# Performance work log

Measured on AMD Instinct MI355X. Metric: run time of the kernel, lower is better.

The kernel has to match this reference:

```python
import jax, jax.numpy as jnp
import numpy as np

N_NODES = 100000
N_EDGES = 1000000
D_FEAT = 64          # per-node embedding dim
IN_FEATS = 2 * D_FEAT  # concat(src, dst)
HID = 128


def setup_inputs() -> dict:
    key = jax.random.key(0)
    ks = jax.random.split(key, 12)
    zi = jax.random.normal(ks[0], (N_NODES, D_FEAT), dtype=jnp.float32)
    zj = jax.random.normal(ks[1], (N_NODES, D_FEAT), dtype=jnp.float32)
    zn = jax.random.normal(ks[2], (N_NODES, D_FEAT), dtype=jnp.float32)
    pos_src = jax.random.randint(ks[3], (N_EDGES,), 0, N_NODES)
    pos_dst = jax.random.randint(ks[4], (N_EDGES,), 0, N_NODES)
    neg_src = jax.random.randint(ks[5], (N_EDGES,), 0, N_NODES)
    neg_dst = jax.random.randint(ks[6], (N_EDGES,), 0, N_NODES)
    # MLP params (nn.Linear style: y = x @ W.T + b)
    s1 = 1.0 / np.sqrt(IN_FEATS)
    s3 = 1.0 / np.sqrt(HID)
    W1 = jax.random.uniform(ks[7], (HID, IN_FEATS), jnp.float32, -s1, s1)
    b1 = jax.random.uniform(ks[8], (HID,), jnp.float32, -s1, s1)
    W3 = jax.random.uniform(ks[9], (1, HID), jnp.float32, -s3, s3)
    b3 = jax.random.uniform(ks[10], (1,), jnp.float32, -s3, s3)
    return {"zi": zi, "zj": zj, "zn": zn, "W1": W1, "b1": b1, "W3": W3,
            "b3": b3, "pos_src": pos_src, "pos_dst": pos_dst,
            "neg_src": neg_src, "neg_dst": neg_dst}


def _lp(raw, W1, b1, W3, b3):
    # Link_Prediction with n_layers=2, dropout=0: linear-relu-linear-sigmoid
    hid = jax.nn.relu(raw @ W1.T + b1)      # [E, HID]
    return jax.nn.sigmoid(hid @ W3.T + b3)  # [E, 1]


def reference(zi, zj, zn, W1, b1, W3, b3, pos_src, pos_dst, neg_src, neg_dst):
    # pos graph: gather src/dst node embeddings per edge, concat -> MLP
    raw_pos = jnp.concatenate([zi[pos_src], zj[pos_dst]], axis=1)  # [E, 2*D]
    pos_score = _lp(raw_pos, W1, b1, W3, b3)
    # NOTE: source bug — neg score is computed from the POS raw features
    # (pos_graph.edata['raw']); the neg gather/concat is dead code, so we
    # faithfully score raw_pos again.
    neg_score = _lp(raw_pos, W1, b1, W3, b3)
    return pos_score, neg_score
```

## Files before the change

### kernel.cpp

```cpp
#include <hip/hip_runtime.h>
#include <hip/hip_fp8.h>

typedef float    f32x16 __attribute__((ext_vector_type(16)));
typedef _Float16 f16x8  __attribute__((ext_vector_type(8)));
typedef long     i64;

#define NWAVES 4
#define TPW 4
#define TILES_PER_BLOCK (NWAVES * TPW)
#define W1_LDS 32768

__device__ __forceinline__ uint32_t enc4_fp8(float a, float b, float c, float d) {
#if __has_builtin(__builtin_amdgcn_cvt_pk_fp8_f32)
    int w = __builtin_amdgcn_cvt_pk_fp8_f32(a, b, 0, false);
    w     = __builtin_amdgcn_cvt_pk_fp8_f32(c, d, w, true);
    return (uint32_t)w;
#else
    __hip_fp8_e4m3 e0(a), e1(b), e2(c), e3(d);
    return (uint32_t)e0.__x | ((uint32_t)e1.__x << 8) |
           ((uint32_t)e2.__x << 16) | ((uint32_t)e3.__x << 24);
#endif
}

__device__ __forceinline__ void dec4_fp8f(uint32_t w, float* o) {
#if __has_builtin(__builtin_amdgcn_cvt_pk_f32_fp8)
    const auto f01 = __builtin_amdgcn_cvt_pk_f32_fp8((int)w, false);
    const auto f23 = __builtin_amdgcn_cvt_pk_f32_fp8((int)w, true);
    o[0] = f01[0]; o[1] = f01[1]; o[2] = f23[0]; o[3] = f23[1];
#else
    #pragma unroll
    for (int j = 0; j < 4; ++j) {
        __hip_fp8_e4m3 t; t.__x = (unsigned char)(w >> (8 * j));
        o[j] = (float)t;
    }
#endif
}

__device__ __forceinline__ i64 mk64(uint32_t lo, uint32_t hi) {
    return (i64)(((unsigned long long)hi << 32) | (unsigned long long)lo);
}

__device__ __forceinline__ void gl_lds16(const void* g, void* l) {
    __builtin_amdgcn_global_load_lds(
        (const __attribute__((address_space(1))) void*)g,
        (__attribute__((address_space(3))) void*)l, 16, 0, 0);
}

__global__ __launch_bounds__(256) void prep_fp8(
    const float* __restrict__ zi, const float* __restrict__ zj,
    uint2* __restrict__ zif8, uint2* __restrict__ zjf8, const int nChunkPer)
{
    const int stride = gridDim.x * blockDim.x;
    for (int c = blockIdx.x * blockDim.x + threadIdx.x; c < 2 * nChunkPer; c += stride) {
        const float* s;
        uint2* d;
        int cc;
        if (c < nChunkPer) { cc = c; s = zi + (size_t)cc * 8; d = zif8 + cc; }
        else { cc = c - nChunkPer; s = zj + (size_t)cc * 8; d = zjf8 + cc; }
        const float4 a0 = *reinterpret_cast<const float4*>(s);
        const float4 a1 = *reinterpret_cast<const float4*>(s + 4);
        uint2 w;
        w.x = enc4_fp8(a0.x, a0.y, a0.z, a0.w);
        w.y = enc4_fp8(a1.x, a1.y, a1.z, a1.w);
        *d = w;
    }
}

__global__ __launch_bounds__(256) void prep_w1(
    const float* __restrict__ W1, uint4* __restrict__ w1pack)
{
    const int c = blockIdx.x * blockDim.x + threadIdx.x;
    if (c >= 2048) return;
    const int n  = c >> 4, q = c & 15;
    const int kk = q >> 1, lq = q & 1;
    const int kbase = (kk < 4) ? (lq * 32 + kk * 8) : (64 + lq * 32 + (kk - 4) * 8);
    const float* w = W1 + n * 128 + kbase;
    const float4 w0 = *reinterpret_cast<const float4*>(w);
    const float4 w1 = *reinterpret_cast<const float4*>(w + 4);
    const uint32_t h0 = enc4_fp8(w0.x, w0.y, w0.z, w0.w);
    const uint32_t h1 = enc4_fp8(w1.x, w1.y, w1.z, w1.w);
    float d0[4], d1[4];
    dec4_fp8f(h0, d0);
    dec4_fp8f(h1, d1);
    const uint32_t r0 = enc4_fp8((w0.x - d0[0]) * 16.0f, (w0.y - d0[1]) * 16.0f,
                                 (w0.z - d0[2]) * 16.0f, (w0.w - d0[3]) * 16.0f);
    const uint32_t r1 = enc4_fp8((w1.x - d1[0]) * 16.0f, (w1.y - d1[1]) * 16.0f,
                                 (w1.z - d1[2]) * 16.0f, (w1.w - d1[3]) * 16.0f);
    uint4 o; o.x = h0; o.y = h1; o.z = r0; o.w = r1;
    w1pack[c] = o;
}

template<bool FP8>
__global__ __launch_bounds__(256) void graphlp_mfma(
    const float* __restrict__ zi, const float* __restrict__ zj,
    const unsigned char* __restrict__ zif8, const unsigned char* __restrict__ zjf8,
    const uint4* __restrict__ w1pack,
    const float* __restrict__ W1, const float* __restrict__ b1p,
    const float* __restrict__ W3, const float* __restrict__ b3p,
    const int* __restrict__ psrc, const int* __restrict__ pdst,
    float* __restrict__ out, const int nEdges, const int nTiles)
{
    __shared__ char ldsbuf[65536];
    char* lds = ldsbuf;
    const int tid = threadIdx.x;

    if constexpr (FP8) {
        #pragma unroll
        for (int i = 0; i < 8; ++i) {
            const int ch = tid + i * 256;
            const int n  = ch >> 4;
            const int q  = ch & 15;
            const uint4 v = w1pack[ch];
            const int off = n * 256 + ((q * 16) ^ ((n & 7) << 4));
            *reinterpret_cast<uint4*>(lds + off) = v;
        }
    } else {
        #pragma unroll
        for (int i = 0; i < 8; ++i) {
            const int ch  = tid + i * 256;
            const int row = ch >> 4;
            const int kg  = ch & 15;
            const float* s = W1 + row * 128 + kg * 8;
            const float4 a0 = *reinterpret_cast<const float4*>(s);
            const float4 a1 = *reinterpret_cast<const float4*>(s + 4);
            f16x8 v;
            v[0]=(_Float16)a0.x; v[1]=(_Float16)a0.y; v[2]=(_Float16)a0.z; v[3]=(_Float16)a0.w;
            v[4]=(_Float16)a1.x; v[5]=(_Float16)a1.y; v[6]=(_Float16)a1.z; v[7]=(_Float16)a1.w;
            const int off = row * 256 + ((kg * 16) ^ ((row & 7) << 4));
            *reinterpret_cast<f16x8*>(lds + off) = v;
        }
    }
    __syncthreads();

    const int lane = tid & 63;
    const int wav  = tid >> 6;
    const int lr   = lane & 31;
    const int lq   = lane >> 5;

    float b1v[4], w3v[4];
    #pragma unroll
    for (int nb = 0; nb < 4; ++nb) {
        b1v[nb] = b1p[nb * 32 + lr];
        w3v[nb] = W3[nb * 32 + lr];
    }
    const float b3 = b3p[0];

    const int nT1 = nTiles - 1;
    const int gb  = blockIdx.x * TILES_PER_BLOCK + wav;

    if constexpr (FP8) {
        int sia[TPW], dia[TPW];
        #pragma unroll
        for (int t = 0; t < TPW; ++t) {
            const int gt = min(gb + t * NWAVES, nT1);
            const int et = min(gt * 32 + lr, nEdges - 1);
            sia[t] = psrc[et];
            dia[t] = pdst[et];
        }
        char* stage = ldsbuf + W1_LDS + wav * 8192;
        {
            const unsigned char* sp = zif8 + (size_t)sia[0] * 64 + lq * 16;
            const unsigned char* dp = zjf8 + (size_t)dia[0] * 64 + lq * 16;
            gl_lds16(sp,      stage);
            gl_lds16(sp + 32, stage + 1024);
            gl_lds16(dp,      stage + 2048);
            gl_lds16(dp + 32, stage + 3072);
        }

        #pragma unroll
        for (int t = 0; t < TPW; ++t) {
            const int g = min(gb + t * NWAVES, nT1);

            {
                const int tn = (t + 1 < TPW) ? (t + 1) : t;
                char* dst = stage + ((t + 1) & 1) * 4096;
                const unsigned char* sp = zif8 + (size_t)sia[tn] * 64 + lq * 16;
                const unsigned char* dp = zjf8 + (size_t)dia[tn] * 64 + lq * 16;
                gl_lds16(sp,      dst);
                gl_lds16(sp + 32, dst + 1024);
                gl_lds16(dp,      dst + 2048);
                gl_lds16(dp + 32, dst + 3072);
            }

            if (t == 0) asm volatile("s_waitcnt vmcnt(4)" ::: "memory");
            else        asm volatile("s_waitcnt vmcnt(5)" ::: "memory");
            __builtin_amdgcn_sched_barrier(0);

            const char* rb = stage + (t & 1) * 4096 + lq * 1024 + lr * 16;
            const uint4 as0 = *reinterpret_cast<const uint4*>(rb);
            const uint4 as1 = *reinterpret_cast<const uint4*>(rb + 512);
            const uint4 ad0 = *reinterpret_cast<const uint4*>(rb + 2048);
            const uint4 ad1 = *reinterpret_cast<const uint4*>(rb + 2560);
            i64 aop[8];
            aop[0] = mk64(as0.x, as0.y); aop[1] = mk64(as0.z, as0.w);
            aop[2] = mk64(as1.x, as1.y); aop[3] = mk64(as1.z, as1.w);
            aop[4] = mk64(ad0.x, ad0.y); aop[5] = mk64(ad0.z, ad0.w);
            aop[6] = mk64(ad1.x, ad1.y); aop[7] = mk64(ad1.z, ad1.w);

            float pr[16];
            #pragma unroll
            for (int r = 0; r < 16; ++r) pr[r] = 0.0f;

            #pragma unroll
            for (int nb = 0; nb < 4; ++nb) {
                const float bb = b1v[nb];
                f32x16 acc, accr;
                #pragma unroll
                for (int r = 0; r < 16; ++r) { acc[r] = bb; accr[r] = 0.0f; }
                const int n   = nb * 32 + lr;
                const int nsw = (n & 7) << 4;
                const int nbase = n * 256;
                __builtin_amdgcn_s_setprio(1);
                #pragma unroll
                for (int kk = 0; kk < 8; ++kk) {
                    const int off = nbase + (((kk * 2 + lq) * 16) ^ nsw);
                    const uint4 w = *reinterpret_cast<const uint4*>(lds + off);
                    acc  = __builtin_amdgcn_mfma_f32_32x32x16_fp8_fp8(
                               aop[kk], mk64(w.x, w.y), acc,  0, 0, 0);
                    accr = __builtin_amdgcn_mfma_f32_32x32x16_fp8_fp8(
                               aop[kk], mk64(w.z, w.w), accr, 0, 0, 0);
                }
                __builtin_amdgcn_s_setprio(0);
                const float ww = w3v[nb];
                #pragma unroll
                for (int r = 0; r < 16; ++r) {
                    const float h = fmaf(accr[r], 0.0625f, acc[r]);
                    pr[r] = fmaf(fmaxf(h, 0.0f), ww, pr[r]);
                }
            }

            float p8[8];
            #pragma unroll
            for (int r = 0; r < 8; ++r) {
                const float lo = pr[r], hi = pr[r + 8];
                const float sent = (lane & 1) ? lo : hi;
                const float got  = __shfl_xor(sent, 1);
                p8[r] = ((lane & 1) ? hi : lo) + got;
            }
            float p4[4];
            #pragma unroll
            for (int r = 0; r < 4; ++r) {
                const float lo = p8[r], hi = p8[r + 4];
                const float sent = (lane & 2) ? lo : hi;
                const float got  = __shfl_xor(sent, 2);
                p4[r] = ((lane & 2) ? hi : lo) + got;
            }
            float p2[2];
            #pragma unroll
            for (int r = 0; r < 2; ++r) {
                const float lo = p4[r], hi = p4[r + 2];
                const float sent = (lane & 4) ? lo : hi;
                const float got  = __shfl_xor(sent, 4);
                p2[r] = ((lane & 4) ? hi : lo) + got;
            }
            float p1;
            {
                const float lo = p2[0], hi = p2[1];
                const float sent = (lane & 8) ? lo : hi;
                const float got  = __shfl_xor(sent, 8);
                p1 = ((lane & 8) ? hi : lo) + got;
            }
            p1 += __shfl_xor(p1, 16);

            const int rid = 8 * (lane & 1) + 4 * ((lane >> 1) & 1)
                          + 2 * ((lane >> 2) & 1) + ((lane >> 3) & 1);
            const int m  = (rid & 3) + 8 * (rid >> 2) + 4 * lq;
            const int eoc = min(g * 32 + m, nEdges - 1);
            const float sc = 1.0f / (1.0f + __expf(-(p1 + b3)));
            out[(lane & 16) ? (nEdges + eoc) : eoc] = sc;
        }
    } else {
        int si = 0, di = 0;
        {
            const int g0 = gb;
            if (g0 < nTiles) {
                const int e = min(g0 * 32 + lr, nEdges - 1);
                si = psrc[e]; di = pdst[e];
            }
        }
        for (int t = 0; t < TPW; ++t) {
            const int g = gb + t * NWAVES;
            if (g >= nTiles) break;
            int si_n = 0, di_n = 0;
            if (t + 1 < TPW) {
                const int gn = g + NWAVES;
                if (gn < nTiles) {
                    const int en = min(gn * 32 + lr, nEdges - 1);
                    si_n = psrc[en]; di_n = pdst[en];
                }
            }
            f16x8 afrag[8];
            const float* __restrict__ sp = zi + (size_t)si * 64;
            const float* __restrict__ dp = zj + (size_t)di * 64;
            #pragma unroll
            for (int kk = 0; kk < 8; ++kk) {
                const int kb = kk * 16 + lq * 8;
                const float* p = (kk < 4) ? (sp + kb) : (dp + kb - 64);
                const float4 a0 = *reinterpret_cast<const float4*>(p);
                const float4 a1 = *reinterpret_cast<const float4*>(p + 4);
                f16x8 v;
                v[0]=(_Float16)a0.x; v[1]=(_Float16)a0.y; v[2]=(_Float16)a0.z; v[3]=(_Float16)a0.w;
                v[4]=(_Float16)a1.x; v[5]=(_Float16)a1.y; v[6]=(_Float16)a1.z; v[7]=(_Float16)a1.w;
                afrag[kk] = v;
            }
            float pr[16];
            #pragma unroll
            for (int r = 0; r < 16; ++r) pr[r] = 0.0f;
            #pragma unroll
            for (int nbp = 0; nbp < 2; ++nbp) {
                const float bb0 = b1v[2*nbp], bb1 = b1v[2*nbp + 1];
                f32x16 acc0, acc1;
                #pragma unroll
                for (int r = 0; r < 16; ++r) { acc0[r] = bb0; acc1[r] = bb1; }
                const int n0 = (2*nbp)     * 32 + lr;
                const int n1 = (2*nbp + 1) * 32 + lr;
                #pragma unroll
                for (int kk = 0; kk < 8; ++kk) {
                    const int kx = kk * 32 + lq * 16;
                    const f16x8 bf0 = *reinterpret_cast<const f16x8*>(
                        lds + n0 * 256 + (kx ^ ((n0 & 7) << 4)));
                    const f16x8 bf1 = *reinterpret_cast<const f16x8*>(
                        lds + n1 * 256 + (kx ^ ((n1 & 7) << 4)));
                    acc0 = __builtin_amdgcn_mfma_f32_32x32x16_f16(afrag[kk], bf0, acc0, 0, 0, 0);
                    acc1 = __builtin_amdgcn_mfma_f32_32x32x16_f16(afrag[kk], bf1, acc1, 0, 0, 0);
                }
                const float ww0 = w3v[2*nbp], ww1 = w3v[2*nbp + 1];
                #pragma unroll
                for (int r = 0; r < 16; ++r) {
                    pr[r] = fmaf(fmaxf(acc0[r], 0.0f), ww0, pr[r]);
                    pr[r] = fmaf(fmaxf(acc1[r], 0.0f), ww1, pr[r]);
                }
            }
            float p8[8];
            #pragma unroll
            for (int r = 0; r < 8; ++r) {
                const float lo = pr[r], hi = pr[r + 8];
                const float sent = (lane & 1) ? lo : hi;
                const float got  = __shfl_xor(sent, 1);
                p8[r] = ((lane & 1) ? hi : lo) + got;
            }
            float p4[4];
            #pragma unroll
            for (int r = 0; r < 4; ++r) {
                const float lo = p8[r], hi = p8[r + 4];
                const float sent = (lane & 2) ? lo : hi;
                const float got  = __shfl_xor(sent, 2);
                p4[r] = ((lane & 2) ? hi : lo) + got;
            }
            float p2[2];
            #pragma unroll
            for (int r = 0; r < 2; ++r) {
                const float lo = p4[r], hi = p4[r + 2];
                const float sent = (lane & 4) ? lo : hi;
                const float got  = __shfl_xor(sent, 4);
                p2[r] = ((lane & 4) ? hi : lo) + got;
            }
            float p1;
            {
                const float lo = p2[0], hi = p2[1];
                const float sent = (lane & 8) ? lo : hi;
                const float got  = __shfl_xor(sent, 8);
                p1 = ((lane & 8) ? hi : lo) + got;
            }
            p1 += __shfl_xor(p1, 16);
            const int rid = 8 * (lane & 1) + 4 * ((lane >> 1) & 1)
                          + 2 * ((lane >> 2) & 1) + ((lane >> 3) & 1);
            const int m  = (rid & 3) + 8 * (rid >> 2) + 4 * lq;
            const int eo = g * 32 + m;
            if (eo < nEdges) {
                const float sc = 1.0f / (1.0f + __expf(-(p1 + b3)));
                if (lane & 16) out[nEdges + eo] = sc;
                else           out[eo] = sc;
            }
            si = si_n; di = di_n;
        }
    }
}

extern "C" void kernel_launch(void* const* d_in, const int* in_sizes, int n_in,
                              void* d_out, int out_size, void* d_ws, size_t ws_size,
                              hipStream_t stream)
{
    const float* zi = (const float*)d_in[0];
    const float* zj = (const float*)d_in[1];
    const float* W1 = (const float*)d_in[3];
    const float* b1 = (const float*)d_in[4];
    const float* W3 = (const float*)d_in[5];
    const float* b3 = (const float*)d_in[6];
    const int* psrc = (const int*)d_in[7];
    const int* pdst = (const int*)d_in[8];
    float* out = (float*)d_out;

    const int nEdges = in_sizes[7];
    const int nNodesI = in_sizes[0] / 64;
    const int nNodesJ = in_sizes[1] / 64;
    const int nTiles = (nEdges + 31) / 32;
    const int nBlocks = (nTiles + TILES_PER_BLOCK - 1) / TILES_PER_BLOCK;

    const size_t bytesI = (size_t)nNodesI * 64;
    const size_t bytesJ = (size_t)nNodesJ * 64;
    const size_t bytesW = 2048 * 16;
    const bool useF8 = (ws_size >= bytesI + bytesJ + bytesW);

    if (useF8) {
        unsigned char* zif8 = (unsigned char*)d_ws;
        unsigned char* zjf8 = (unsigned char*)d_ws + bytesI;
        uint4* w1pack = (uint4*)((unsigned char*)d_ws + bytesI + bytesJ);
        const int nChunkPer = nNodesI * 64 / 8;
        hipLaunchKernelGGL(prep_fp8, dim3(2048), dim3(256), 0, stream,
                           zi, zj, (uint2*)zif8, (uint2*)zjf8, nChunkPer);
        hipLaunchKernelGGL(prep_w1, dim3(8), dim3(256), 0, stream, W1, w1pack);
        hipLaunchKernelGGL((graphlp_mfma<true>), dim3(nBlocks), dim3(256), 0, stream,
                           zi, zj, zif8, zjf8, w1pack, W1, b1, W3, b3, psrc, pdst,
                           out, nEdges, nTiles);
    } else {
        hipLaunchKernelGGL((graphlp_mfma<false>), dim3(nBlocks), dim3(256), 0, stream,
                           zi, zj, (const unsigned char*)nullptr, (const unsigned char*)nullptr,
                           (const uint4*)nullptr, W1, b1, W3, b3, psrc, pdst,
                           out, nEdges, nTiles);
    }
}
```

Baseline: 78.47 us.

## Replace LDS-staged async gathers with register double-buffered direct global loads

```diff
diff --git a/kernel.cpp b/kernel.cpp
--- a/kernel.cpp
+++ b/kernel.cpp
@@ -8,7 +8,6 @@
 #define NWAVES 4
 #define TPW 4
 #define TILES_PER_BLOCK (NWAVES * TPW)
-#define W1_LDS 32768
 
 __device__ __forceinline__ uint32_t enc4_fp8(float a, float b, float c, float d) {
 #if __has_builtin(__builtin_amdgcn_cvt_pk_fp8_f32)
@@ -38,12 +37,6 @@
 
 __device__ __forceinline__ i64 mk64(uint32_t lo, uint32_t hi) {
     return (i64)(((unsigned long long)hi << 32) | (unsigned long long)lo);
-}
-
-__device__ __forceinline__ void gl_lds16(const void* g, void* l) {
-    __builtin_amdgcn_global_load_lds(
-        (const __attribute__((address_space(1))) void*)g,
-        (__attribute__((address_space(3))) void*)l, 16, 0, 0);
 }
 
 __global__ __launch_bounds__(256) void prep_fp8(
@@ -100,8 +93,8 @@
     const int* __restrict__ psrc, const int* __restrict__ pdst,
     float* __restrict__ out, const int nEdges, const int nTiles)
 {
-    __shared__ char ldsbuf[65536];
-    char* lds = ldsbuf;
+    __shared__ uint4 w1s[2048];
+    char* lds = reinterpret_cast<char*>(w1s);
     const int tid = threadIdx.x;
 
     if constexpr (FP8) {
@@ -149,53 +142,50 @@
     const int gb  = blockIdx.x * TILES_PER_BLOCK + wav;
 
     if constexpr (FP8) {
-        int sia[TPW], dia[TPW];
-        #pragma unroll
-        for (int t = 0; t < TPW; ++t) {
-            const int gt = min(gb + t * NWAVES, nT1);
-            const int et = min(gt * 32 + lr, nEdges - 1);
-            sia[t] = psrc[et];
-            dia[t] = pdst[et];
-        }
-        char* stage = ldsbuf + W1_LDS + wav * 8192;
+        uint2 px[8];
+        int si1, di1;
         {
-            const unsigned char* sp = zif8 + (size_t)sia[0] * 64 + lq * 16;
-            const unsigned char* dp = zjf8 + (size_t)dia[0] * 64 + lq * 16;
-            gl_lds16(sp,      stage);
-            gl_lds16(sp + 32, stage + 1024);
-            gl_lds16(dp,      stage + 2048);
-            gl_lds16(dp + 32, stage + 3072);
+            const int g0 = min(gb, nT1);
+            const int e0 = min(g0 * 32 + lr, nEdges - 1);
+            const int si0 = psrc[e0], di0 = pdst[e0];
+            const int g1 = min(gb + NWAVES, nT1);
+            const int e1 = min(g1 * 32 + lr, nEdges - 1);
+            si1 = psrc[e1]; di1 = pdst[e1];
+            const unsigned char* sp = zif8 + (size_t)si0 * 64 + lq * 32;
+            const unsigned char* dp = zjf8 + (size_t)di0 * 64 + lq * 32;
+            const uint4 s0 = *reinterpret_cast<const uint4*>(sp);
+            const uint4 s1 = *reinterpret_cast<const uint4*>(sp + 16);
+            const uint4 d0 = *reinterpret_cast<const uint4*>(dp);
+            const uint4 d1 = *reinterpret_cast<const uint4*>(dp + 16);
+            px[0].x=s0.x; px[0].y=s0.y; px[1].x=s0.z; px[1].y=s0.w;
+            px[2].x=s1.x; px[2].y=s1.y; px[3].x=s1.z; px[3].y=s1.w;
+            px[4].x=d0.x; px[4].y=d0.y; px[5].x=d0.z; px[5].y=d0.w;
+            px[6].x=d1.x; px[6].y=d1.y; px[7].x=d1.z; px[7].y=d1.w;
         }
 
         #pragma unroll
         for (int t = 0; t < TPW; ++t) {
             const int g = min(gb + t * NWAVES, nT1);
 
+            uint2 pn[8];
             {
-                const int tn = (t + 1 < TPW) ? (t + 1) : t;
-                char* dst = stage + ((t + 1) & 1) * 4096;
-                const unsigned char* sp = zif8 + (size_t)sia[tn] * 64 + lq * 16;
-                const unsigned char* dp = zjf8 + (size_t)dia[tn] * 64 + lq * 16;
-                gl_lds16(sp,      dst);
-                gl_lds16(sp + 32, dst + 1024);
-                gl_lds16(dp,      dst + 2048);
-                gl_lds16(dp + 32, dst + 3072);
-            }
-
-            if (t == 0) asm volatile("s_waitcnt vmcnt(4)" ::: "memory");
-            else        asm volatile("s_waitcnt vmcnt(5)" ::: "memory");
-            __builtin_amdgcn_sched_barrier(0);
-
-            const char* rb = stage + (t & 1) * 4096 + lq * 1024 + lr * 16;
-            const uint4 as0 = *reinterpret_cast<const uint4*>(rb);
-            const uint4 as1 = *reinterpret_cast<const uint4*>(rb + 512);
-            const uint4 ad0 = *reinterpret_cast<const uint4*>(rb + 2048);
-            const uint4 ad1 = *reinterpret_cast<const uint4*>(rb + 2560);
-            i64 aop[8];
-            aop[0] = mk64(as0.x, as0.y); aop[1] = mk64(as0.z, as0.w);
-            aop[2] = mk64(as1.x, as1.y); aop[3] = mk64(as1.z, as1.w);
-            aop[4] = mk64(ad0.x, ad0.y); aop[5] = mk64(ad0.z, ad0.w);
-            aop[6] = mk64(ad1.x, ad1.y); aop[7] = mk64(ad1.z, ad1.w);
+                const unsigned char* sp = zif8 + (size_t)si1 * 64 + lq * 32;
+                const unsigned char* dp = zjf8 + (size_t)di1 * 64 + lq * 32;
+                const uint4 s0 = *reinterpret_cast<const uint4*>(sp);
+                const uint4 s1 = *reinterpret_cast<const uint4*>(sp + 16);
+                const uint4 d0 = *reinterpret_cast<const uint4*>(dp);
+                const uint4 d1 = *reinterpret_cast<const uint4*>(dp + 16);
+                pn[0].x=s0.x; pn[0].y=s0.y; pn[1].x=s0.z; pn[1].y=s0.w;
+                pn[2].x=s1.x; pn[2].y=s1.y; pn[3].x=s1.z; pn[3].y=s1.w;
+                pn[4].x=d0.x; pn[4].y=d0.y; pn[5].x=d0.z; pn[5].y=d0.w;
+                pn[6].x=d1.x; pn[6].y=d1.y; pn[7].x=d1.z; pn[7].y=d1.w;
+            }
+            int si2, di2;
+            {
+                const int g2 = min(gb + (t + 2) * NWAVES, nT1);
+                const int e2 = min(g2 * 32 + lr, nEdges - 1);
+                si2 = psrc[e2]; di2 = pdst[e2];
+            }
 
             float pr[16];
             #pragma unroll
@@ -215,10 +205,11 @@
                 for (int kk = 0; kk < 8; ++kk) {
                     const int off = nbase + (((kk * 2 + lq) * 16) ^ nsw);
                     const uint4 w = *reinterpret_cast<const uint4*>(lds + off);
+                    const i64 a = mk64(px[kk].x, px[kk].y);
                     acc  = __builtin_amdgcn_mfma_f32_32x32x16_fp8_fp8(
-                               aop[kk], mk64(w.x, w.y), acc,  0, 0, 0);
+                               a, mk64(w.x, w.y), acc,  0, 0, 0);
                     accr = __builtin_amdgcn_mfma_f32_32x32x16_fp8_fp8(
-                               aop[kk], mk64(w.z, w.w), accr, 0, 0, 0);
+                               a, mk64(w.z, w.w), accr, 0, 0, 0);
                 }
                 __builtin_amdgcn_s_setprio(0);
                 const float ww = w3v[nb];
@@ -265,16 +256,19 @@
             const int rid = 8 * (lane & 1) + 4 * ((lane >> 1) & 1)
                           + 2 * ((lane >> 2) & 1) + ((lane >> 3) & 1);
             const int m  = (rid & 3) + 8 * (rid >> 2) + 4 * lq;
-            const int eoc = min(g * 32 + m, nEdges - 1);
+            const int eo = min(g * 32 + m, nEdges - 1);
             const float sc = 1.0f / (1.0f + __expf(-(p1 + b3)));
-            out[(lane & 16) ? (nEdges + eoc) : eoc] = sc;
+            out[(lane & 16) ? (nEdges + eo) : eo] = sc;
+
+            #pragma unroll
+            for (int kk = 0; kk < 8; ++kk) px[kk] = pn[kk];
+            si1 = si2; di1 = di2;
         }
     } else {
         int si = 0, di = 0;
         {
-            const int g0 = gb;
-            if (g0 < nTiles) {
-                const int e = min(g0 * 32 + lr, nEdges - 1);
+            if (gb < nTiles) {
+                const int e = min(gb * 32 + lr, nEdges - 1);
                 si = psrc[e]; di = pdst[e];
             }
         }
```

New measurement: 75.38 us. -3.9%, faster.
